# Performance work log

Measured on AMD Instinct MI355X. Metric: run time of the kernel, lower is better.

The kernel has to match this reference:

```python
import jax, jax.numpy as jnp
import numpy as np

GAMMA = 0.1
NUM_STEPS = 50
EPSILON = 1e-06


def setup_inputs() -> dict:
    key = jax.random.key(0)
    k1, k2, k3 = jax.random.split(key, 3)
    n, m = 8192, 8192
    C = jax.random.uniform(k1, (n, m), dtype=jnp.float32)
    d = jax.random.uniform(k2, (n,), dtype=jnp.float32)
    s = jax.random.uniform(k3, (m,), dtype=jnp.float32)
    return {"C": C, "d": d, "s": s}


def reference(C, d, s):
    log_d = jnp.log(d + EPSILON)  # [n]
    log_s = jnp.log(s + EPSILON)  # [m]
    M = -C / GAMMA                # [n, m]
    u0 = jnp.ones_like(log_d)
    v0 = jnp.ones_like(log_s)

    def step(carry, _):
        u, v = carry
        u = log_d - jax.nn.logsumexp(M + v[None, :], axis=1)  # [n]
        v = log_s - jax.nn.logsumexp(M + u[:, None], axis=0)  # [m]
        return (u, v), None

    (u, v), _ = jax.lax.scan(step, (u0, v0), None, length=NUM_STEPS)
    P = u[:, None] + M + v[None, :]
    return jnp.exp(P)
```

## Files before the change

kernel.cpp:

```cpp
#include <hip/hip_runtime.h>
#include <math.h>

#define EPS   1e-6f
#define NDIM  8192
#define NSTEPS 50
#define SCALE (-14.426950408889634f)
#define KLOG2 8.0f
#define KSCALE 256.0f
#define GPAD 12

typedef float v2f __attribute__((ext_vector_type(2)));
typedef float v4f __attribute__((ext_vector_type(4)));

__device__ __forceinline__ v2f cvt2lo(unsigned w) {
  return __builtin_amdgcn_cvt_pk_f32_fp8(w, false);
}
__device__ __forceinline__ v2f cvt2hi(unsigned w) {
  return __builtin_amdgcn_cvt_pk_f32_fp8(w, true);
}

__global__ __launch_bounds__(1024) void prologue_k(const float4* __restrict__ C,
                                                   uint2* __restrict__ K8) {
  int tid = blockIdx.x * 1024 + threadIdx.x;
  v4f c0 = __builtin_nontemporal_load((const v4f*)C + (size_t)tid * 2);
  v4f c1 = __builtin_nontemporal_load((const v4f*)C + (size_t)tid * 2 + 1);
  unsigned lo = 0, hi = 0;
  lo = __builtin_amdgcn_cvt_pk_fp8_f32(exp2f(c0.x * SCALE + KLOG2),
                                       exp2f(c0.y * SCALE + KLOG2), lo, false);
  lo = __builtin_amdgcn_cvt_pk_fp8_f32(exp2f(c0.z * SCALE + KLOG2),
                                       exp2f(c0.w * SCALE + KLOG2), lo, true);
  hi = __builtin_amdgcn_cvt_pk_fp8_f32(exp2f(c1.x * SCALE + KLOG2),
                                       exp2f(c1.y * SCALE + KLOG2), hi, false);
  hi = __builtin_amdgcn_cvt_pk_fp8_f32(exp2f(c1.z * SCALE + KLOG2),
                                       exp2f(c1.w * SCALE + KLOG2), hi, true);
  uint2 o; o.x = lo; o.y = hi;
  K8[tid] = o;
}

template <bool USEK>
__global__ __launch_bounds__(1024) void phaseA_k(const void* __restrict__ Kp,
                                                 const float* __restrict__ zprev,
                                                 const float* __restrict__ s,
                                                 const float* __restrict__ d,
                                                 float* __restrict__ a,
                                                 float* __restrict__ zcur) {
  __shared__ float bs[1024 * GPAD];
  int t = threadIdx.x;
  {
    float4 ba, bb;
    if (zprev) {
      const float4* zp4 = (const float4*)zprev;
      const float4* s4 = (const float4*)s;
      float4 za = zp4[2 * t], zb = zp4[2 * t + 1];
      float4 sa = s4[2 * t], sb = s4[2 * t + 1];
      ba.x = (sa.x + EPS) / za.x; ba.y = (sa.y + EPS) / za.y;
      ba.z = (sa.z + EPS) / za.z; ba.w = (sa.w + EPS) / za.w;
      bb.x = (sb.x + EPS) / zb.x; bb.y = (sb.y + EPS) / zb.y;
      bb.z = (sb.z + EPS) / zb.z; bb.w = (sb.w + EPS) / zb.w;
    } else {
      const float E = 2.718281828459045f;
      ba = float4{E, E, E, E}; bb = ba;
    }
    *(float4*)&bs[t * GPAD]     = ba;
    *(float4*)&bs[t * GPAD + 4] = bb;
  }
  if (t < 32) zcur[blockIdx.x * 32 + t] = 0.f;
  __syncthreads();

  int wave = t >> 6, lane = t & 63;
  int row0 = blockIdx.x * 32 + wave, row1 = row0 + 16;
  float acc0 = 0.f, acc1 = 0.f;
  if (USEK) {
    const uint2* K0 = (const uint2*)Kp + (size_t)row0 * 1024;
    const uint2* K1 = (const uint2*)Kp + (size_t)row1 * 1024;
    #pragma unroll 4
    for (int k = 0; k < 16; k++) {
      int idx = k * 64 + lane;
      uint2 q0 = K0[idx], q1 = K1[idx];
      const float4* bp = (const float4*)&bs[idx * GPAD];
      float4 b0 = bp[0], b1 = bp[1];
      v2f f;
      f = cvt2lo(q0.x); acc0 += f.x * b0.x + f.y * b0.y;
      f = cvt2hi(q0.x); acc0 += f.x * b0.z + f.y * b0.w;
      f = cvt2lo(q0.y); acc0 += f.x * b1.x + f.y * b1.y;
      f = cvt2hi(q0.y); acc0 += f.x * b1.z + f.y * b1.w;
      f = cvt2lo(q1.x); acc1 += f.x * b0.x + f.y * b0.y;
      f = cvt2hi(q1.x); acc1 += f.x * b0.z + f.y * b0.w;
      f = cvt2lo(q1.y); acc1 += f.x * b1.x + f.y * b1.y;
      f = cvt2hi(q1.y); acc1 += f.x * b1.z + f.y * b1.w;
    }
  } else {
    const float4* C0 = (const float4*)Kp + (size_t)row0 * 2048;
    const float4* C1 = (const float4*)Kp + (size_t)row1 * 2048;
    for (int k = 0; k < 16; k++) {
      int idx = k * 64 + lane;
      const float4* bp = (const float4*)&bs[idx * GPAD];
      float4 b0 = bp[0], b1 = bp[1];
      float4 c0 = C0[idx * 2], c1 = C0[idx * 2 + 1];
      acc0 += exp2f(c0.x * SCALE + KLOG2) * b0.x + exp2f(c0.y * SCALE + KLOG2) * b0.y
            + exp2f(c0.z * SCALE + KLOG2) * b0.z + exp2f(c0.w * SCALE + KLOG2) * b0.w
            + exp2f(c1.x * SCALE + KLOG2) * b1.x + exp2f(c1.y * SCALE + KLOG2) * b1.y
            + exp2f(c1.z * SCALE + KLOG2) * b1.z + exp2f(c1.w * SCALE + KLOG2) * b1.w;
      c0 = C1[idx * 2]; c1 = C1[idx * 2 + 1];
      acc1 += exp2f(c0.x * SCALE + KLOG2) * b0.x + exp2f(c0.y * SCALE + KLOG2) * b0.y
            + exp2f(c0.z * SCALE + KLOG2) * b0.z + exp2f(c0.w * SCALE + KLOG2) * b0.w
            + exp2f(c1.x * SCALE + KLOG2) * b1.x + exp2f(c1.y * SCALE + KLOG2) * b1.y
            + exp2f(c1.z * SCALE + KLOG2) * b1.z + exp2f(c1.w * SCALE + KLOG2) * b1.w;
    }
  }
  #pragma unroll
  for (int off = 32; off; off >>= 1) {
    acc0 += __shfl_down(acc0, off, 64);
    acc1 += __shfl_down(acc1, off, 64);
  }
  if (lane == 0) {
    a[row0] = (d[row0] + EPS) / acc0;
    a[row1] = (d[row1] + EPS) / acc1;
  }
}

template <bool USEK>
__global__ __launch_bounds__(1024) void phaseB_k(const void* __restrict__ Kp,
                                                 const float* __restrict__ a,
                                                 float* __restrict__ zcur) {
  __shared__ float as_[256];
  __shared__ float part[8 * 1024];
  int t = threadIdx.x;
  int cg = blockIdx.x & 7, rg = blockIdx.x >> 3;
  if (t < 256) as_[t] = a[rg * 256 + t];
  __syncthreads();
  int ct = t & 127, rl = t >> 7;
  float acc[8];
  #pragma unroll
  for (int k = 0; k < 8; k++) acc[k] = 0.f;
  int r0 = rg * 256 + rl * 32;
  if (USEK) {
    const uint2* K2 = (const uint2*)Kp;
    int base = cg * 128 + ct;
    #pragma unroll 4
    for (int rr = 0; rr < 32; rr++) {
      uint2 q = K2[(size_t)(r0 + rr) * 1024 + base];
      float av = as_[rl * 32 + rr];
      v2f f;
      f = cvt2lo(q.x); acc[0] += f.x * av; acc[1] += f.y * av;
      f = cvt2hi(q.x); acc[2] += f.x * av; acc[3] += f.y * av;
      f = cvt2lo(q.y); acc[4] += f.x * av; acc[5] += f.y * av;
      f = cvt2hi(q.y); acc[6] += f.x * av; acc[7] += f.y * av;
    }
  } else {
    const float4* Cq = (const float4*)Kp;
    int base = cg * 256 + ct * 2;
    for (int rr = 0; rr < 32; rr++) {
      int r = r0 + rr;
      float4 c0 = Cq[(size_t)r * 2048 + base], c1 = Cq[(size_t)r * 2048 + base + 1];
      float av = as_[rl * 32 + rr];
      acc[0] += exp2f(c0.x * SCALE + KLOG2) * av; acc[1] += exp2f(c0.y * SCALE + KLOG2) * av;
      acc[2] += exp2f(c0.z * SCALE + KLOG2) * av; acc[3] += exp2f(c0.w * SCALE + KLOG2) * av;
      acc[4] += exp2f(c1.x * SCALE + KLOG2) * av; acc[5] += exp2f(c1.y * SCALE + KLOG2) * av;
      acc[6] += exp2f(c1.z * SCALE + KLOG2) * av; acc[7] += exp2f(c1.w * SCALE + KLOG2) * av;
    }
  }
  int sw = ((ct >> 2) & 1) << 2;
  float4 lo4 = {acc[0], acc[1], acc[2], acc[3]};
  float4 hi4 = {acc[4], acc[5], acc[6], acc[7]};
  *(float4*)&part[rl * 1024 + ct * 8 + (0 ^ sw)] = lo4;
  *(float4*)&part[rl * 1024 + ct * 8 + (4 ^ sw)] = hi4;
  __syncthreads();
  int ridx = t ^ (((t >> 5) & 1) << 2);
  float sum = 0.f;
  #pragma unroll
  for (int r2 = 0; r2 < 8; r2++) sum += part[r2 * 1024 + ridx];
  atomicAdd(&zcur[cg * 1024 + t], sum);
}

__global__ __launch_bounds__(1024) void epilogue_k(const float4* __restrict__ C,
                                                   const float* __restrict__ a,
                                                   const float* __restrict__ zlast,
                                                   const float* __restrict__ s,
                                                   float4* __restrict__ out) {
  __shared__ float4 bs4[2048];
  int t = threadIdx.x;
  {
    const float4* s4 = (const float4*)s;
    const float4* z4 = (const float4*)zlast;
    float4 sa = s4[2 * t], sb = s4[2 * t + 1];
    float4 za = z4[2 * t], zb = z4[2 * t + 1];
    float4 ba = {(sa.x + EPS) / za.x, (sa.y + EPS) / za.y,
                 (sa.z + EPS) / za.z, (sa.w + EPS) / za.w};
    float4 bb = {(sb.x + EPS) / zb.x, (sb.y + EPS) / zb.y,
                 (sb.z + EPS) / zb.z, (sb.w + EPS) / zb.w};
    bs4[2 * t] = ba; bs4[2 * t + 1] = bb;
  }
  __syncthreads();
  int wave = t >> 6, lane = t & 63;
  int row = blockIdx.x * 16 + wave;
  float av = a[row] * KSCALE;
  const v4f* Crow = (const v4f*)(C + (size_t)row * 2048);
  v4f* Orow = (v4f*)(out + (size_t)row * 2048);
  for (int k = 0; k < 32; k++) {
    int idx = k * 64 + lane;
    v4f c = __builtin_nontemporal_load(&Crow[idx]);
    float4 bq = bs4[idx];
    v4f p;
    p.x = av * bq.x * exp2f(c.x * SCALE);
    p.y = av * bq.y * exp2f(c.y * SCALE);
    p.z = av * bq.z * exp2f(c.z * SCALE);
    p.w = av * bq.w * exp2f(c.w * SCALE);
    __builtin_nontemporal_store(p, &Orow[idx]);
  }
}

extern "C" void kernel_launch(void* const* d_in, const int* in_sizes, int n_in,
                              void* d_out, int out_size, void* d_ws, size_t ws_size,
                              hipStream_t stream) {
  const float* C = (const float*)d_in[0];
  const float* dd = (const float*)d_in[1];
  const float* ss = (const float*)d_in[2];

  float* z0 = (float*)d_ws;
  float* z1 = z0 + NDIM;
  float* a  = z1 + NDIM;
  char* kbase = (char*)d_ws + 131072;
  size_t kneed = 131072 + (size_t)NDIM * NDIM;
  bool usek = ws_size >= kneed;

  if (usek) {
    prologue_k<<<8192, 1024, 0, stream>>>((const float4*)C, (uint2*)kbase);
  }
  const void* Kp = usek ? (const void*)kbase : (const void*)C;

  for (int it = 0; it < NSTEPS; ++it) {
    float* zc = (it & 1) ? z1 : z0;
    const float* zp = (it == 0) ? nullptr : ((it & 1) ? z0 : z1);
    if (usek) {
      phaseA_k<true><<<256, 1024, 0, stream>>>(Kp, zp, ss, dd, a, zc);
      phaseB_k<true><<<256, 1024, 0, stream>>>(Kp, a, zc);
    } else {
      phaseA_k<false><<<256, 1024, 0, stream>>>(Kp, zp, ss, dd, a, zc);
      phaseB_k<false><<<256, 1024, 0, stream>>>(Kp, a, zc);
    }
  }
  const float* zlast = ((NSTEPS - 1) & 1) ? z1 : z0;
  epilogue_k<<<512, 1024, 0, stream>>>((const float4*)C, a, zlast, ss, (float4*)d_out);
}
```

Baseline: 1.890 ms.

## Fuse all Sinkhorn iterations into one cooperative persistent kernel with grid barriers

Replaces the 100 separate phase-A/phase-B kernel launches with a single cooperative kernel of 256 blocks that loops over all iterations. A software grid barrier (atomic counter plus spin) separates the phases, and shared memory is reused between them. This removes per-launch overhead and the idle gaps between launches, at the cost of barrier spin latency and relaxed atomic loads and stores for the cross-block vectors. The fallback path without the fp8 workspace is split into separate non-templated kernels.

Result: slower. 2.628 ms (+39.1%).

```diff
diff --git a/kernel.cpp b/kernel.cpp
--- a/kernel.cpp
+++ b/kernel.cpp
@@ -8,6 +8,7 @@
 #define KLOG2 8.0f
 #define KSCALE 256.0f
 #define GPAD 12
+#define NBLK 256
 
 typedef float v2f __attribute__((ext_vector_type(2)));
 typedef float v4f __attribute__((ext_vector_type(4)));
@@ -19,9 +20,31 @@
   return __builtin_amdgcn_cvt_pk_f32_fp8(w, true);
 }
 
+__device__ __forceinline__ float aload(const float* p) {
+  return __hip_atomic_load(p, __ATOMIC_RELAXED, __HIP_MEMORY_SCOPE_AGENT);
+}
+__device__ __forceinline__ void astore(float* p, float v) {
+  __hip_atomic_store(p, v, __ATOMIC_RELAXED, __HIP_MEMORY_SCOPE_AGENT);
+}
+
+__device__ __forceinline__ void grid_barrier(unsigned* ctr, unsigned target) {
+  __syncthreads();
+  if (threadIdx.x == 0) {
+    asm volatile("s_waitcnt vmcnt(0)" ::: "memory");
+    __hip_atomic_fetch_add(ctr, 1u, __ATOMIC_RELAXED, __HIP_MEMORY_SCOPE_AGENT);
+    while (__hip_atomic_load(ctr, __ATOMIC_RELAXED, __HIP_MEMORY_SCOPE_AGENT) < target) {
+      __builtin_amdgcn_s_sleep(1);
+    }
+  }
+  __syncthreads();
+}
+
 __global__ __launch_bounds__(1024) void prologue_k(const float4* __restrict__ C,
-                                                   uint2* __restrict__ K8) {
+                                                   uint2* __restrict__ K8,
+                                                   unsigned* __restrict__ ctr) {
   int tid = blockIdx.x * 1024 + threadIdx.x;
+  if (tid == 0)
+    __hip_atomic_store(ctr, 0u, __ATOMIC_RELAXED, __HIP_MEMORY_SCOPE_AGENT);
   v4f c0 = __builtin_nontemporal_load((const v4f*)C + (size_t)tid * 2);
   v4f c1 = __builtin_nontemporal_load((const v4f*)C + (size_t)tid * 2 + 1);
   unsigned lo = 0, hi = 0;
@@ -37,140 +60,112 @@
   K8[tid] = o;
 }
 
-template <bool USEK>
-__global__ __launch_bounds__(1024) void phaseA_k(const void* __restrict__ Kp,
-                                                 const float* __restrict__ zprev,
-                                                 const float* __restrict__ s,
-                                                 const float* __restrict__ d,
-                                                 float* __restrict__ a,
-                                                 float* __restrict__ zcur) {
-  __shared__ float bs[1024 * GPAD];
-  int t = threadIdx.x;
-  {
-    float4 ba, bb;
-    if (zprev) {
-      const float4* zp4 = (const float4*)zprev;
-      const float4* s4 = (const float4*)s;
-      float4 za = zp4[2 * t], zb = zp4[2 * t + 1];
-      float4 sa = s4[2 * t], sb = s4[2 * t + 1];
-      ba.x = (sa.x + EPS) / za.x; ba.y = (sa.y + EPS) / za.y;
-      ba.z = (sa.z + EPS) / za.z; ba.w = (sa.w + EPS) / za.w;
-      bb.x = (sb.x + EPS) / zb.x; bb.y = (sb.y + EPS) / zb.y;
-      bb.z = (sb.z + EPS) / zb.z; bb.w = (sb.w + EPS) / zb.w;
-    } else {
-      const float E = 2.718281828459045f;
-      ba = float4{E, E, E, E}; bb = ba;
-    }
-    *(float4*)&bs[t * GPAD]     = ba;
-    *(float4*)&bs[t * GPAD + 4] = bb;
-  }
-  if (t < 32) zcur[blockIdx.x * 32 + t] = 0.f;
-  __syncthreads();
-
-  int wave = t >> 6, lane = t & 63;
-  int row0 = blockIdx.x * 32 + wave, row1 = row0 + 16;
-  float acc0 = 0.f, acc1 = 0.f;
-  if (USEK) {
-    const uint2* K0 = (const uint2*)Kp + (size_t)row0 * 1024;
-    const uint2* K1 = (const uint2*)Kp + (size_t)row1 * 1024;
-    #pragma unroll 4
-    for (int k = 0; k < 16; k++) {
-      int idx = k * 64 + lane;
-      uint2 q0 = K0[idx], q1 = K1[idx];
-      const float4* bp = (const float4*)&bs[idx * GPAD];
-      float4 b0 = bp[0], b1 = bp[1];
-      v2f f;
-      f = cvt2lo(q0.x); acc0 += f.x * b0.x + f.y * b0.y;
-      f = cvt2hi(q0.x); acc0 += f.x * b0.z + f.y * b0.w;
-      f = cvt2lo(q0.y); acc0 += f.x * b1.x + f.y * b1.y;
-      f = cvt2hi(q0.y); acc0 += f.x * b1.z + f.y * b1.w;
-      f = cvt2lo(q1.x); acc1 += f.x * b0.x + f.y * b0.y;
-      f = cvt2hi(q1.x); acc1 += f.x * b0.z + f.y * b0.w;
-      f = cvt2lo(q1.y); acc1 += f.x * b1.x + f.y * b1.y;
-      f = cvt2hi(q1.y); acc1 += f.x * b1.z + f.y * b1.w;
-    }
-  } else {
-    const float4* C0 = (const float4*)Kp + (size_t)row0 * 2048;
-    const float4* C1 = (const float4*)Kp + (size_t)row1 * 2048;
-    for (int k = 0; k < 16; k++) {
-      int idx = k * 64 + lane;
-      const float4* bp = (const float4*)&bs[idx * GPAD];
-      float4 b0 = bp[0], b1 = bp[1];
-      float4 c0 = C0[idx * 2], c1 = C0[idx * 2 + 1];
-      acc0 += exp2f(c0.x * SCALE + KLOG2) * b0.x + exp2f(c0.y * SCALE + KLOG2) * b0.y
-            + exp2f(c0.z * SCALE + KLOG2) * b0.z + exp2f(c0.w * SCALE + KLOG2) * b0.w
-            + exp2f(c1.x * SCALE + KLOG2) * b1.x + exp2f(c1.y * SCALE + KLOG2) * b1.y
-            + exp2f(c1.z * SCALE + KLOG2) * b1.z + exp2f(c1.w * SCALE + KLOG2) * b1.w;
-      c0 = C1[idx * 2]; c1 = C1[idx * 2 + 1];
-      acc1 += exp2f(c0.x * SCALE + KLOG2) * b0.x + exp2f(c0.y * SCALE + KLOG2) * b0.y
-            + exp2f(c0.z * SCALE + KLOG2) * b0.z + exp2f(c0.w * SCALE + KLOG2) * b0.w
-            + exp2f(c1.x * SCALE + KLOG2) * b1.x + exp2f(c1.y * SCALE + KLOG2) * b1.y
-            + exp2f(c1.z * SCALE + KLOG2) * b1.z + exp2f(c1.w * SCALE + KLOG2) * b1.w;
-    }
-  }
-  #pragma unroll
-  for (int off = 32; off; off >>= 1) {
-    acc0 += __shfl_down(acc0, off, 64);
-    acc1 += __shfl_down(acc1, off, 64);
-  }
-  if (lane == 0) {
-    a[row0] = (d[row0] + EPS) / acc0;
-    a[row1] = (d[row1] + EPS) / acc1;
-  }
-}
-
-template <bool USEK>
-__global__ __launch_bounds__(1024) void phaseB_k(const void* __restrict__ Kp,
-                                                 const float* __restrict__ a,
-                                                 float* __restrict__ zcur) {
-  __shared__ float as_[256];
-  __shared__ float part[8 * 1024];
-  int t = threadIdx.x;
-  int cg = blockIdx.x & 7, rg = blockIdx.x >> 3;
-  if (t < 256) as_[t] = a[rg * 256 + t];
-  __syncthreads();
-  int ct = t & 127, rl = t >> 7;
-  float acc[8];
-  #pragma unroll
-  for (int k = 0; k < 8; k++) acc[k] = 0.f;
-  int r0 = rg * 256 + rl * 32;
-  if (USEK) {
-    const uint2* K2 = (const uint2*)Kp;
-    int base = cg * 128 + ct;
-    #pragma unroll 4
-    for (int rr = 0; rr < 32; rr++) {
-      uint2 q = K2[(size_t)(r0 + rr) * 1024 + base];
-      float av = as_[rl * 32 + rr];
-      v2f f;
-      f = cvt2lo(q.x); acc[0] += f.x * av; acc[1] += f.y * av;
-      f = cvt2hi(q.x); acc[2] += f.x * av; acc[3] += f.y * av;
-      f = cvt2lo(q.y); acc[4] += f.x * av; acc[5] += f.y * av;
-      f = cvt2hi(q.y); acc[6] += f.x * av; acc[7] += f.y * av;
-    }
-  } else {
-    const float4* Cq = (const float4*)Kp;
-    int base = cg * 256 + ct * 2;
-    for (int rr = 0; rr < 32; rr++) {
-      int r = r0 + rr;
-      float4 c0 = Cq[(size_t)r * 2048 + base], c1 = Cq[(size_t)r * 2048 + base + 1];
-      float av = as_[rl * 32 + rr];
-      acc[0] += exp2f(c0.x * SCALE + KLOG2) * av; acc[1] += exp2f(c0.y * SCALE + KLOG2) * av;
-      acc[2] += exp2f(c0.z * SCALE + KLOG2) * av; acc[3] += exp2f(c0.w * SCALE + KLOG2) * av;
-      acc[4] += exp2f(c1.x * SCALE + KLOG2) * av; acc[5] += exp2f(c1.y * SCALE + KLOG2) * av;
-      acc[6] += exp2f(c1.z * SCALE + KLOG2) * av; acc[7] += exp2f(c1.w * SCALE + KLOG2) * av;
-    }
-  }
-  int sw = ((ct >> 2) & 1) << 2;
-  float4 lo4 = {acc[0], acc[1], acc[2], acc[3]};
-  float4 hi4 = {acc[4], acc[5], acc[6], acc[7]};
-  *(float4*)&part[rl * 1024 + ct * 8 + (0 ^ sw)] = lo4;
-  *(float4*)&part[rl * 1024 + ct * 8 + (4 ^ sw)] = hi4;
-  __syncthreads();
-  int ridx = t ^ (((t >> 5) & 1) << 2);
-  float sum = 0.f;
-  #pragma unroll
-  for (int r2 = 0; r2 < 8; r2++) sum += part[r2 * 1024 + ridx];
-  atomicAdd(&zcur[cg * 1024 + t], sum);
+__global__ __launch_bounds__(1024) void fused_k(const uint2* __restrict__ K,
+                                                const float* __restrict__ d,
+                                                const float* __restrict__ s,
+                                                float* z0, float* z1,
+                                                float* a, unsigned* ctr) {
+  __shared__ float smem[12288 + 256];
+  float* bs = smem;
+  float* part = smem;
+  float* as_ = smem + 12288;
+  const int t = threadIdx.x, bid = blockIdx.x;
+  const int wave = t >> 6, lane = t & 63;
+  unsigned bt = 0;
+
+  for (int it = 0; it < NSTEPS; ++it) {
+    float* zc = (it & 1) ? z1 : z0;
+    float* zp = (it & 1) ? z0 : z1;
+
+    {
+      float4 ba, bb;
+      if (it == 0) {
+        const float E = 2.718281828459045f;
+        ba = float4{E, E, E, E}; bb = ba;
+      } else {
+        const float4* s4 = (const float4*)s;
+        float4 sa = s4[2 * t], sb = s4[2 * t + 1];
+        float z8[8];
+        #pragma unroll
+        for (int k = 0; k < 8; k++) z8[k] = aload(&zp[8 * t + k]);
+        ba.x = (sa.x + EPS) / z8[0]; ba.y = (sa.y + EPS) / z8[1];
+        ba.z = (sa.z + EPS) / z8[2]; ba.w = (sa.w + EPS) / z8[3];
+        bb.x = (sb.x + EPS) / z8[4]; bb.y = (sb.y + EPS) / z8[5];
+        bb.z = (sb.z + EPS) / z8[6]; bb.w = (sb.w + EPS) / z8[7];
+      }
+      *(float4*)&bs[t * GPAD]     = ba;
+      *(float4*)&bs[t * GPAD + 4] = bb;
+    }
+    if (t < 32) astore(&zc[bid * 32 + t], 0.f);
+    __syncthreads();
+
+    {
+      int row0 = bid * 32 + wave, row1 = row0 + 16;
+      const uint2* K0 = K + (size_t)row0 * 1024;
+      const uint2* K1 = K + (size_t)row1 * 1024;
+      float acc0 = 0.f, acc1 = 0.f;
+      #pragma unroll 4
+      for (int k = 0; k < 16; k++) {
+        int idx = k * 64 + lane;
+        uint2 q0 = K0[idx], q1 = K1[idx];
+        const float4* bp = (const float4*)&bs[idx * GPAD];
+        float4 b0 = bp[0], b1 = bp[1];
+        v2f f;
+        f = cvt2lo(q0.x); acc0 += f.x * b0.x + f.y * b0.y;
+        f = cvt2hi(q0.x); acc0 += f.x * b0.z + f.y * b0.w;
+        f = cvt2lo(q0.y); acc0 += f.x * b1.x + f.y * b1.y;
+        f = cvt2hi(q0.y); acc0 += f.x * b1.z + f.y * b1.w;
+        f = cvt2lo(q1.x); acc1 += f.x * b0.x + f.y * b0.y;
+        f = cvt2hi(q1.x); acc1 += f.x * b0.z + f.y * b0.w;
+        f = cvt2lo(q1.y); acc1 += f.x * b1.x + f.y * b1.y;
+        f = cvt2hi(q1.y); acc1 += f.x * b1.z + f.y * b1.w;
+      }
+      #pragma unroll
+      for (int off = 32; off; off >>= 1) {
+        acc0 += __shfl_down(acc0, off, 64);
+        acc1 += __shfl_down(acc1, off, 64);
+      }
+      if (lane == 0) {
+        astore(&a[row0], (d[row0] + EPS) / acc0);
+        astore(&a[row1], (d[row1] + EPS) / acc1);
+      }
+    }
+    grid_barrier(ctr, (++bt) * NBLK);
+
+    {
+      int cg = bid & 7, rg = bid >> 3;
+      if (t < 256) as_[t] = aload(&a[rg * 256 + t]);
+      __syncthreads();
+      int ct = t & 127, rl = t >> 7;
+      float acc[8];
+      #pragma unroll
+      for (int k = 0; k < 8; k++) acc[k] = 0.f;
+      int r0 = rg * 256 + rl * 32;
+      int base = cg * 128 + ct;
+      #pragma unroll 4
+      for (int rr = 0; rr < 32; rr++) {
+        uint2 q = K[(size_t)(r0 + rr) * 1024 + base];
+        float av = as_[rl * 32 + rr];
+        v2f f;
+        f = cvt2lo(q.x); acc[0] += f.x * av; acc[1] += f.y * av;
+        f = cvt2hi(q.x); acc[2] += f.x * av; acc[3] += f.y * av;
+        f = cvt2lo(q.y); acc[4] += f.x * av; acc[5] += f.y * av;
+        f = cvt2hi(q.y); acc[6] += f.x * av; acc[7] += f.y * av;
+      }
+      int sw = ((ct >> 2) & 1) << 2;
+      float4 lo4 = {acc[0], acc[1], acc[2], acc[3]};
+      float4 hi4 = {acc[4], acc[5], acc[6], acc[7]};
+      *(float4*)&part[rl * 1024 + ct * 8 + (0 ^ sw)] = lo4;
+      *(float4*)&part[rl * 1024 + ct * 8 + (4 ^ sw)] = hi4;
+      __syncthreads();
+      int ridx = t ^ (((t >> 5) & 1) << 2);
+      float sum = 0.f;
+      #pragma unroll
+      for (int r2 = 0; r2 < 8; r2++) sum += part[r2 * 1024 + ridx];
+      atomicAdd(&zc[cg * 1024 + t], sum);
+    }
+    grid_barrier(ctr, (++bt) * NBLK);
+  }
 }
 
 __global__ __launch_bounds__(1024) void epilogue_k(const float4* __restrict__ C,
@@ -210,6 +205,123 @@
   }
 }
 
+__global__ __launch_bounds__(1024) void phaseA_c(const float4* __restrict__ C,
+                                                 const float* __restrict__ zprev,
+                                                 const float* __restrict__ s,
+                                                 const float* __restrict__ d,
+                                                 float* __restrict__ a,
+                                                 float* __restrict__ zcur) {
+  __shared__ float bs[NDIM];
+  int t = threadIdx.x;
+  float4* bs4 = (float4*)bs;
+  if (zprev) {
+    const float4* zp4 = (const float4*)zprev;
+    const float4* s4 = (const float4*)s;
+    float4 za = zp4[2 * t], zb = zp4[2 * t + 1];
+    float4 sa = s4[2 * t], sb = s4[2 * t + 1];
+    float4 ba = {(sa.x + EPS) / za.x, (sa.y + EPS) / za.y,
+                 (sa.z + EPS) / za.z, (sa.w + EPS) / za.w};
+    float4 bb = {(sb.x + EPS) / zb.x, (sb.y + EPS) / zb.y,
+                 (sb.z + EPS) / zb.z, (sb.w + EPS) / zb.w};
+    bs4[2 * t] = ba; bs4[2 * t + 1] = bb;
+  } else {
+    const float E = 2.718281828459045f;
+    float4 e4 = {E, E, E, E};
+    bs4[2 * t] = e4; bs4[2 * t + 1] = e4;
+  }
+  if (t < 32) zcur[blockIdx.x * 32 + t] = 0.f;
+  __syncthreads();
+  int wave = t >> 6, lane = t & 63;
+  for (int rr = wave; rr < 32; rr += 16) {
+    int row = blockIdx.x * 32 + rr;
+    const float4* Cq = C + (size_t)row * 2048;
+    float acc = 0.f;
+    for (int k = 0; k < 16; k++) {
+      int idx = k * 64 + lane;
+      float4 c0 = Cq[idx * 2], c1 = Cq[idx * 2 + 1];
+      const float4* bp = (const float4*)&bs[idx * 8];
+      float4 b0 = bp[0], b1 = bp[1];
+      acc += exp2f(c0.x * SCALE) * b0.x + exp2f(c0.y * SCALE) * b0.y
+           + exp2f(c0.z * SCALE) * b0.z + exp2f(c0.w * SCALE) * b0.w
+           + exp2f(c1.x * SCALE) * b1.x + exp2f(c1.y * SCALE) * b1.y
+           + exp2f(c1.z * SCALE) * b1.z + exp2f(c1.w * SCALE) * b1.w;
+    }
+    #pragma unroll
+    for (int off = 32; off; off >>= 1) acc += __shfl_down(acc, off, 64);
+    if (lane == 0) a[row] = (d[row] + EPS) / acc;
+  }
+}
+
+__global__ __launch_bounds__(1024) void phaseB_c(const float4* __restrict__ C,
+                                                 const float* __restrict__ a,
+                                                 float* __restrict__ zcur) {
+  __shared__ float as_[256];
+  __shared__ float part[8192];
+  int t = threadIdx.x;
+  int cg = blockIdx.x & 7, rg = blockIdx.x >> 3;
+  if (t < 256) as_[t] = a[rg * 256 + t];
+  __syncthreads();
+  int ct = t & 127, rl = t >> 7;
+  float acc[8];
+  #pragma unroll
+  for (int k = 0; k < 8; k++) acc[k] = 0.f;
+  int base = cg * 256 + ct * 2;
+  for (int rr = 0; rr < 32; rr++) {
+    int r = rg * 256 + rl * 32 + rr;
+    float4 c0 = C[(size_t)r * 2048 + base], c1 = C[(size_t)r * 2048 + base + 1];
+    float av = as_[rl * 32 + rr];
+    acc[0] += exp2f(c0.x * SCALE) * av; acc[1] += exp2f(c0.y * SCALE) * av;
+    acc[2] += exp2f(c0.z * SCALE) * av; acc[3] += exp2f(c0.w * SCALE) * av;
+    acc[4] += exp2f(c1.x * SCALE) * av; acc[5] += exp2f(c1.y * SCALE) * av;
+    acc[6] += exp2f(c1.z * SCALE) * av; acc[7] += exp2f(c1.w * SCALE) * av;
+  }
+  float* pp = &part[rl * 1024 + ct * 8];
+  #pragma unroll
+  for (int k = 0; k < 8; k++) pp[k] = acc[k];
+  __syncthreads();
+  float sum = 0.f;
+  #pragma unroll
+  for (int r2 = 0; r2 < 8; r2++) sum += part[r2 * 1024 + t];
+  atomicAdd(&zcur[cg * 1024 + t], sum);
+}
+
+__global__ __launch_bounds__(1024) void epilogue_c(const float4* __restrict__ C,
+                                                   const float* __restrict__ a,
+                                                   const float* __restrict__ zlast,
+                                                   const float* __restrict__ s,
+                                                   float4* __restrict__ out) {
+  __shared__ float4 bs4[2048];
+  int t = threadIdx.x;
+  {
+    const float4* s4 = (const float4*)s;
+    const float4* z4 = (const float4*)zlast;
+    float4 sa = s4[2 * t], sb = s4[2 * t + 1];
+    float4 za = z4[2 * t], zb = z4[2 * t + 1];
+    float4 ba = {(sa.x + EPS) / za.x, (sa.y + EPS) / za.y,
+                 (sa.z + EPS) / za.z, (sa.w + EPS) / za.w};
+    float4 bb = {(sb.x + EPS) / zb.x, (sb.y + EPS) / zb.y,
+                 (sb.z + EPS) / zb.z, (sb.w + EPS) / zb.w};
+    bs4[2 * t] = ba; bs4[2 * t + 1] = bb;
+  }
+  __syncthreads();
+  int wave = t >> 6, lane = t & 63;
+  int row = blockIdx.x * 16 + wave;
+  float av = a[row];
+  const v4f* Crow = (const v4f*)(C + (size_t)row * 2048);
+  v4f* Orow = (v4f*)(out + (size_t)row * 2048);
+  for (int k = 0; k < 32; k++) {
+    int idx = k * 64 + lane;
+    v4f c = __builtin_nontemporal_load(&Crow[idx]);
+    float4 bq = bs4[idx];
+    v4f p;
+    p.x = av * bq.x * exp2f(c.x * SCALE);
+    p.y = av * bq.y * exp2f(c.y * SCALE);
+    p.z = av * bq.z * exp2f(c.z * SCALE);
+    p.w = av * bq.w * exp2f(c.w * SCALE);
+    __builtin_nontemporal_store(p, &Orow[idx]);
+  }
+}
+
 extern "C" void kernel_launch(void* const* d_in, const int* in_sizes, int n_in,
                               void* d_out, int out_size, void* d_ws, size_t ws_size,
                               hipStream_t stream) {
@@ -220,26 +332,31 @@
   float* z0 = (float*)d_ws;
   float* z1 = z0 + NDIM;
   float* a  = z1 + NDIM;
+  unsigned* ctr = (unsigned*)((char*)d_ws + 98304);
   char* kbase = (char*)d_ws + 131072;
   size_t kneed = 131072 + (size_t)NDIM * NDIM;
   bool usek = ws_size >= kneed;
 
   if (usek) {
-    prologue_k<<<8192, 1024, 0, stream>>>((const float4*)C, (uint2*)kbase);
-  }
-  const void* Kp = usek ? (const void*)kbase : (const void*)C;
-
-  for (int it = 0; it < NSTEPS; ++it) {
-    float* zc = (it & 1) ? z1 : z0;
-    const float* zp = (it == 0) ? nullptr : ((it & 1) ? z0 : z1);
-    if (usek) {
-      phaseA_k<true><<<256, 1024, 0, stream>>>(Kp, zp, ss, dd, a, zc);
-      phaseB_k<true><<<256, 1024, 0, stream>>>(Kp, a, zc);
-    } else {
-      phaseA_k<false><<<256, 1024, 0, stream>>>(Kp, zp, ss, dd, a, zc);
-      phaseB_k<false><<<256, 1024, 0, stream>>>(Kp, a, zc);
-    }
-  }
-  const float* zlast = ((NSTEPS - 1) & 1) ? z1 : z0;
-  epilogue_k<<<512, 1024, 0, stream>>>((const float4*)C, a, zlast, ss, (float4*)d_out);
-}
+    uint2* K8 = (uint2*)kbase;
+    prologue_k<<<8192, 1024, 0, stream>>>((const float4*)C, K8, ctr);
+    const uint2* Kp = K8;
+    void* kargs[] = {(void*)&Kp, (void*)&dd, (void*)&ss,
+                     (void*)&z0, (void*)&z1, (void*)&a, (void*)&ctr};
+    hipLaunchCooperativeKernel((void*)fused_k, dim3(NBLK), dim3(1024),
+                               kargs, 0, stream);
+    const float* zlast = ((NSTEPS - 1) & 1) ? z1 : z0;
+    epilogue_k<<<512, 1024, 0, stream>>>((const float4*)C, a, zlast, ss,
+                                         (float4*)d_out);
+  } else {
+    for (int it = 0; it < NSTEPS; ++it) {
+      float* zc = (it & 1) ? z1 : z0;
+      const float* zp = (it == 0) ? nullptr : ((it & 1) ? z0 : z1);
+      phaseA_c<<<256, 1024, 0, stream>>>((const float4*)C, zp, ss, dd, a, zc);
+      phaseB_c<<<256, 1024, 0, stream>>>((const float4*)C, a, zc);
+    }
+    const float* zlast = ((NSTEPS - 1) & 1) ? z1 : z0;
+    epilogue_c<<<512, 1024, 0, stream>>>((const float4*)C, a, zlast, ss,
+                                         (float4*)d_out);
+  }
+}
```
